# Optimization experiments

Measured on AMD Instinct MI355X. Metric: run time of the kernel, lower is better.

Reference implementation:

```python
import jax, jax.numpy as jnp
import numpy as np

B_, I_, H_ = 4096, 2048, 2048


def setup_inputs() -> dict:
    key = jax.random.key(0)
    ks = jax.random.split(key, 7)
    x = jax.random.normal(ks[0], (B_, I_), dtype=jnp.float32)
    h = jax.random.normal(ks[1], (B_, H_), dtype=jnp.float32)
    c = jax.random.normal(ks[2], (B_, H_), dtype=jnp.float32)
    n = jax.random.uniform(ks[3], (B_, H_), dtype=jnp.float32)  # positive normalizer state
    m = jax.random.normal(ks[4], (B_, H_), dtype=jnp.float32)
    # xavier_uniform over [I+H, 4H]
    fan_in, fan_out = I_ + H_, 4 * H_
    limit = float(np.sqrt(6.0 / (fan_in + fan_out)))
    W = jax.random.uniform(ks[5], (fan_in, fan_out), dtype=jnp.float32, minval=-limit, maxval=limit)
    Bias = jnp.zeros((fan_out,), dtype=jnp.float32)
    return {"x": x, "h": h, "c": c, "n": n, "m": m, "W": W, "Bias": Bias}


def reference(x, h, c, n, m, W, Bias):
    H = h.shape[1]
    combined = jnp.concatenate([x, h], axis=1)            # [B, I+H]
    gates = combined @ W + Bias                           # [B, 4H]
    z_tilda, i_tilda, f_tilda, o_tilda = jnp.split(gates, 4, axis=1)
    z_t = jnp.tanh(z_tilda)
    f_t = jax.nn.sigmoid(f_tilda)
    o_t = jax.nn.sigmoid(o_tilda)
    # log(sigmoid(f_tilda)) == log_sigmoid(f_tilda); log(exp(i_tilda)) == i_tilda
    m_t = jnp.maximum(jax.nn.log_sigmoid(f_tilda) + m, i_tilda)
    i_prime = jnp.exp(i_tilda - m_t)
    c_t = f_t * c + i_prime * z_t
    n_t = f_t * n + i_prime
    h_t = o_t * (c_t / n_t)
    return jnp.stack([h_t, c_t, n_t, m_t])  # [4, B, H]
```

## Files before the change

kernel.cpp:

```cpp
#include <hip/hip_runtime.h>
#include <hip/hip_fp16.h>

#define B_SZ 4096
#define I_SZ 2048
#define H_SZ 2048
#define K_SZ 4096
#define N_SZ 8192

typedef _Float16 half8_t __attribute__((ext_vector_type(8)));
typedef _Float16 half4_t __attribute__((ext_vector_type(4)));
typedef float    f32x4   __attribute__((ext_vector_type(4)));

typedef const void __attribute__((address_space(1)))* gas_ptr;
typedef void       __attribute__((address_space(3)))* las_ptr;

__device__ __forceinline__ void async_load16(const void* g, void* l) {
    __builtin_amdgcn_global_load_lds((gas_ptr)g, (las_ptr)l, 16, 0, 0);
}

__global__ void cast_combined_kernel(const float* __restrict__ x,
                                     const float* __restrict__ h,
                                     _Float16* __restrict__ A) {
    int idx = blockIdx.x * 256 + threadIdx.x;
    int b   = idx >> 10;
    int c4  = idx & 1023;
    const float* src = (c4 < 512) ? (x + (size_t)b * I_SZ + c4 * 4)
                                  : (h + (size_t)b * H_SZ + (c4 - 512) * 4);
    f32x4 v = *(const f32x4*)src;
    half4_t o = { (_Float16)v[0], (_Float16)v[1], (_Float16)v[2], (_Float16)v[3] };
    *(half4_t*)(A + (size_t)b * K_SZ + c4 * 4) = o;
}

__global__ void transpose_cast_W(const float* __restrict__ W,
                                 _Float16* __restrict__ Wt) {
    __shared__ _Float16 tile[64][65];
    int nt = blockIdx.x;
    int kt = blockIdx.y;
    int tx = threadIdx.x & 63;
    int tg = threadIdx.x >> 6;
#pragma unroll
    for (int r = 0; r < 16; ++r) {
        int kl = r * 4 + tg;
        float v = W[(size_t)(kt * 64 + kl) * N_SZ + nt * 64 + tx];
        tile[kl][tx] = (_Float16)v;
    }
    __syncthreads();
#pragma unroll
    for (int r = 0; r < 16; ++r) {
        int nl = r * 4 + tg;
        Wt[(size_t)(nt * 64 + nl) * K_SZ + kt * 64 + tx] = tile[tx][nl];
    }
}

__global__ __launch_bounds__(256)
void gemm_kernel(const _Float16* __restrict__ A,
                 const _Float16* __restrict__ Wt,
                 float* __restrict__ G) {
    __shared__ _Float16 sA[128 * 32];
    __shared__ _Float16 sB[128 * 32];
    const int t    = threadIdx.x;
    const int wave = t >> 6;
    const int lane = t & 63;
    const int m0 = blockIdx.y * 128;
    const int n0 = blockIdx.x * 128;
    const int wm = (wave >> 1) * 64;
    const int wn = (wave & 1) * 64;

    f32x4 acc[4][4] = {};

    const int srow = wave * 16 + (lane >> 2);
    const int scol = (lane & 3) * 8;
    const _Float16* gA0 = A  + (size_t)(m0 + srow) * K_SZ + scol;
    const _Float16* gB0 = Wt + (size_t)(n0 + srow) * K_SZ + scol;
    char* lA = (char*)sA + wave * 1024;
    char* lB = (char*)sB + wave * 1024;

    const int lm = lane & 15;
    const int kq = (lane >> 4) * 8;

    for (int k0 = 0; k0 < K_SZ; k0 += 32) {
        async_load16(gA0 + k0,             lA);
        async_load16(gA0 + 64 * K_SZ + k0, lA + 4096);
        async_load16(gB0 + k0,             lB);
        async_load16(gB0 + 64 * K_SZ + k0, lB + 4096);
        __syncthreads();

        half8_t af[4], bf[4];
#pragma unroll
        for (int i = 0; i < 4; ++i)
            af[i] = *(const half8_t*)(sA + (wm + i * 16 + lm) * 32 + kq);
#pragma unroll
        for (int i = 0; i < 4; ++i)
            bf[i] = *(const half8_t*)(sB + (wn + i * 16 + lm) * 32 + kq);
#pragma unroll
        for (int mi = 0; mi < 4; ++mi)
#pragma unroll
            for (int ni = 0; ni < 4; ++ni)
                acc[mi][ni] = __builtin_amdgcn_mfma_f32_16x16x32_f16(
                    af[mi], bf[ni], acc[mi][ni], 0, 0, 0);
        __syncthreads();
    }

    const int cr = (lane >> 4) * 4;
    const int cc = lane & 15;
#pragma unroll
    for (int mi = 0; mi < 4; ++mi)
#pragma unroll
        for (int ni = 0; ni < 4; ++ni)
#pragma unroll
            for (int r = 0; r < 4; ++r) {
                int row = m0 + wm + mi * 16 + cr + r;
                int col = n0 + wn + ni * 16 + cc;
                G[(size_t)row * N_SZ + col] = acc[mi][ni][r];
            }
}

__global__ void eltwise_kernel(const float* __restrict__ G,
                               const float* __restrict__ Bias,
                               const float* __restrict__ c,
                               const float* __restrict__ n,
                               const float* __restrict__ m,
                               float* __restrict__ out) {
    const size_t BH = (size_t)B_SZ * H_SZ;
    int idx = blockIdx.x * 256 + threadIdx.x;
    int b  = idx >> 9;
    int j4 = (idx & 511) * 4;
    const float* gr = G + (size_t)b * N_SZ;
    f32x4 zt = *(const f32x4*)(gr + j4);
    f32x4 it = *(const f32x4*)(gr + H_SZ + j4);
    f32x4 ft = *(const f32x4*)(gr + 2 * H_SZ + j4);
    f32x4 ot = *(const f32x4*)(gr + 3 * H_SZ + j4);
    f32x4 bz = *(const f32x4*)(Bias + j4);
    f32x4 bi = *(const f32x4*)(Bias + H_SZ + j4);
    f32x4 bf = *(const f32x4*)(Bias + 2 * H_SZ + j4);
    f32x4 bo = *(const f32x4*)(Bias + 3 * H_SZ + j4);
    f32x4 cv = *(const f32x4*)(c + (size_t)b * H_SZ + j4);
    f32x4 nv = *(const f32x4*)(n + (size_t)b * H_SZ + j4);
    f32x4 mv = *(const f32x4*)(m + (size_t)b * H_SZ + j4);
    f32x4 hR, cR, nR, mR;
#pragma unroll
    for (int q = 0; q < 4; ++q) {
        float z  = zt[q] + bz[q];
        float i  = it[q] + bi[q];
        float f  = ft[q] + bf[q];
        float o  = ot[q] + bo[q];
        float z_t = tanhf(z);
        float f_t = 1.0f / (1.0f + expf(-f));
        float o_t = 1.0f / (1.0f + expf(-o));
        float ls  = fminf(f, 0.0f) - log1pf(expf(-fabsf(f)));
        float m_t = fmaxf(ls + mv[q], i);
        float ip  = expf(i - m_t);
        float c_t = f_t * cv[q] + ip * z_t;
        float n_t = f_t * nv[q] + ip;
        float h_t = o_t * (c_t / n_t);
        hR[q] = h_t; cR[q] = c_t; nR[q] = n_t; mR[q] = m_t;
    }
    size_t off = (size_t)b * H_SZ + j4;
    *(f32x4*)(out + off)          = hR;
    *(f32x4*)(out + BH + off)     = cR;
    *(f32x4*)(out + 2 * BH + off) = nR;
    *(f32x4*)(out + 3 * BH + off) = mR;
}

extern "C" void kernel_launch(void* const* d_in, const int* in_sizes, int n_in,
                              void* d_out, int out_size, void* d_ws, size_t ws_size,
                              hipStream_t stream) {
    const float* x    = (const float*)d_in[0];
    const float* h    = (const float*)d_in[1];
    const float* c    = (const float*)d_in[2];
    const float* n    = (const float*)d_in[3];
    const float* m    = (const float*)d_in[4];
    const float* W    = (const float*)d_in[5];
    const float* Bias = (const float*)d_in[6];
    float* out = (float*)d_out;

    const size_t WT_BYTES = (size_t)N_SZ * K_SZ * 2;
    const size_t A_BYTES  = (size_t)B_SZ * K_SZ * 2;
    const size_t G_BYTES  = (size_t)B_SZ * N_SZ * 4;
    if (ws_size < WT_BYTES + A_BYTES + G_BYTES) return;

    char* ws = (char*)d_ws;
    _Float16* Wt = (_Float16*)ws;
    _Float16* A  = (_Float16*)(ws + WT_BYTES);
    float*    G  = (float*)(ws + WT_BYTES + A_BYTES);

    cast_combined_kernel<<<16384, 256, 0, stream>>>(x, h, A);
    transpose_cast_W<<<dim3(128, 64), 256, 0, stream>>>(W, Wt);
    gemm_kernel<<<dim3(64, 32), 256, 0, stream>>>(A, Wt, G);
    eltwise_kernel<<<8192, 256, 0, stream>>>(G, Bias, c, n, m, out);
}
```

Measured before the change: 813.3 us.

## Fuse LSTM gate epilogue into GEMM with gate-interleaved tiles and swizzled LDS

Each GEMM block now computes the z/i/f/o gate columns for the same 32 hidden units, so the elementwise xLSTM update runs in the GEMM epilogue. This removes the fp32 gates buffer write and re-read and the separate elementwise launch. It also XOR-swizzles the LDS layout to reduce bank conflicts and switches to fast hardware exp2/rcp/log intrinsics, which lowers precision slightly. The W transpose kernel is simplified to a direct strided gather with 8-wide fp16 stores; its uncoalesced reads may cost more than the old shared-memory tile version.

```diff
diff --git a/kernel.cpp b/kernel.cpp
--- a/kernel.cpp
+++ b/kernel.cpp
@@ -1,7 +1,7 @@
 #include <hip/hip_runtime.h>
 #include <hip/hip_fp16.h>
 
-#define B_SZ 4096
+#define M_SZ 4096
 #define I_SZ 2048
 #define H_SZ 2048
 #define K_SZ 4096
@@ -16,6 +16,14 @@
 
 __device__ __forceinline__ void async_load16(const void* g, void* l) {
     __builtin_amdgcn_global_load_lds((gas_ptr)g, (las_ptr)l, 16, 0, 0);
+}
+
+__device__ __forceinline__ float fexp(float x) {
+    return __builtin_amdgcn_exp2f(x * 1.44269504088896340736f);
+}
+__device__ __forceinline__ float frcp(float x) { return __builtin_amdgcn_rcpf(x); }
+__device__ __forceinline__ float flog1p(float t) {
+    return __builtin_amdgcn_logf(1.0f + t) * 0.69314718055994530942f;
 }
 
 __global__ void cast_combined_kernel(const float* __restrict__ x,
@@ -33,69 +41,73 @@
 
 __global__ void transpose_cast_W(const float* __restrict__ W,
                                  _Float16* __restrict__ Wt) {
-    __shared__ _Float16 tile[64][65];
-    int nt = blockIdx.x;
-    int kt = blockIdx.y;
-    int tx = threadIdx.x & 63;
-    int tg = threadIdx.x >> 6;
+    int t  = threadIdx.x;
+    int n  = blockIdx.x * 64 + (t >> 2);
+    int k0 = blockIdx.y * 32 + (t & 3) * 8;
+    half8_t v;
 #pragma unroll
-    for (int r = 0; r < 16; ++r) {
-        int kl = r * 4 + tg;
-        float v = W[(size_t)(kt * 64 + kl) * N_SZ + nt * 64 + tx];
-        tile[kl][tx] = (_Float16)v;
-    }
-    __syncthreads();
-#pragma unroll
-    for (int r = 0; r < 16; ++r) {
-        int nl = r * 4 + tg;
-        Wt[(size_t)(nt * 64 + nl) * K_SZ + kt * 64 + tx] = tile[tx][nl];
-    }
+    for (int j = 0; j < 8; ++j)
+        v[j] = (_Float16)W[(size_t)(k0 + j) * N_SZ + n];
+    *(half8_t*)(Wt + (size_t)n * K_SZ + k0) = v;
 }
 
 __global__ __launch_bounds__(256)
-void gemm_kernel(const _Float16* __restrict__ A,
-                 const _Float16* __restrict__ Wt,
-                 float* __restrict__ G) {
+void gemm_fused_kernel(const _Float16* __restrict__ A,
+                       const _Float16* __restrict__ Wt,
+                       const float* __restrict__ Bias,
+                       const float* __restrict__ Cst,
+                       const float* __restrict__ Nst,
+                       const float* __restrict__ Mst,
+                       float* __restrict__ out) {
     __shared__ _Float16 sA[128 * 32];
     __shared__ _Float16 sB[128 * 32];
     const int t    = threadIdx.x;
     const int wave = t >> 6;
     const int lane = t & 63;
     const int m0 = blockIdx.y * 128;
-    const int n0 = blockIdx.x * 128;
-    const int wm = (wave >> 1) * 64;
-    const int wn = (wave & 1) * 64;
+    const int j0 = blockIdx.x * 32;
 
-    f32x4 acc[4][4] = {};
+    f32x4 acc[2][8] = {};
 
-    const int srow = wave * 16 + (lane >> 2);
-    const int scol = (lane & 3) * 8;
-    const _Float16* gA0 = A  + (size_t)(m0 + srow) * K_SZ + scol;
-    const _Float16* gB0 = Wt + (size_t)(n0 + srow) * K_SZ + scol;
-    char* lA = (char*)sA + wave * 1024;
-    char* lB = (char*)sB + wave * 1024;
+    const int srl   = lane >> 2;
+    const int chunk = (lane & 3) ^ ((lane >> 3) & 3);
+    const int ar0 = wave * 16 + srl;
+    const int br0 = wave * 16 + srl;
+    const int br1 = br0 + 64;
+    const int wrow0 = (br0 >> 5) * H_SZ + j0 + (br0 & 31);
+    const int wrow1 = (br1 >> 5) * H_SZ + j0 + (br1 & 31);
 
-    const int lm = lane & 15;
-    const int kq = (lane >> 4) * 8;
+    const _Float16* gA0 = A  + (size_t)(m0 + ar0) * K_SZ + chunk * 8;
+    const _Float16* gA1 = gA0 + (size_t)64 * K_SZ;
+    const _Float16* gB0 = Wt + (size_t)wrow0 * K_SZ + chunk * 8;
+    const _Float16* gB1 = Wt + (size_t)wrow1 * K_SZ + chunk * 8;
+    char* lA0 = (char*)sA + wave * 1024;
+    char* lA1 = lA0 + 4096;
+    char* lB0 = (char*)sB + wave * 1024;
+    char* lB1 = lB0 + 4096;
+
+    const int lm   = lane & 15;
+    const int slot = (lane >> 4) ^ ((lm >> 1) & 3);
+    const _Float16* fA = sA + (wave * 32 + lm) * 32 + slot * 8;
+    const _Float16* fB = sB + lm * 32 + slot * 8;
 
     for (int k0 = 0; k0 < K_SZ; k0 += 32) {
-        async_load16(gA0 + k0,             lA);
-        async_load16(gA0 + 64 * K_SZ + k0, lA + 4096);
-        async_load16(gB0 + k0,             lB);
-        async_load16(gB0 + 64 * K_SZ + k0, lB + 4096);
+        async_load16(gA0 + k0, lA0);
+        async_load16(gA1 + k0, lA1);
+        async_load16(gB0 + k0, lB0);
+        async_load16(gB1 + k0, lB1);
         __syncthreads();
 
-        half8_t af[4], bf[4];
+        half8_t af[2], bf[8];
+        af[0] = *(const half8_t*)(fA);
+        af[1] = *(const half8_t*)(fA + 16 * 32);
 #pragma unroll
-        for (int i = 0; i < 4; ++i)
-            af[i] = *(const half8_t*)(sA + (wm + i * 16 + lm) * 32 + kq);
+        for (int ni = 0; ni < 8; ++ni)
+            bf[ni] = *(const half8_t*)(fB + ni * 16 * 32);
 #pragma unroll
-        for (int i = 0; i < 4; ++i)
-            bf[i] = *(const half8_t*)(sB + (wn + i * 16 + lm) * 32 + kq);
+        for (int mi = 0; mi < 2; ++mi)
 #pragma unroll
-        for (int mi = 0; mi < 4; ++mi)
-#pragma unroll
-            for (int ni = 0; ni < 4; ++ni)
+            for (int ni = 0; ni < 8; ++ni)
                 acc[mi][ni] = __builtin_amdgcn_mfma_f32_16x16x32_f16(
                     af[mi], bf[ni], acc[mi][ni], 0, 0, 0);
         __syncthreads();
@@ -103,63 +115,40 @@
 
     const int cr = (lane >> 4) * 4;
     const int cc = lane & 15;
+    const size_t bh = (size_t)M_SZ * H_SZ;
 #pragma unroll
-    for (int mi = 0; mi < 4; ++mi)
+    for (int mi = 0; mi < 2; ++mi) {
 #pragma unroll
-        for (int ni = 0; ni < 4; ++ni)
+        for (int nj = 0; nj < 2; ++nj) {
+            const int j = j0 + nj * 16 + cc;
+            const float bz = Bias[j];
+            const float bi = Bias[H_SZ + j];
+            const float bff = Bias[2 * H_SZ + j];
+            const float bo = Bias[3 * H_SZ + j];
 #pragma unroll
             for (int r = 0; r < 4; ++r) {
-                int row = m0 + wm + mi * 16 + cr + r;
-                int col = n0 + wn + ni * 16 + cc;
-                G[(size_t)row * N_SZ + col] = acc[mi][ni][r];
+                const int m = m0 + wave * 32 + mi * 16 + cr + r;
+                const size_t off = (size_t)m * H_SZ + j;
+                float z = acc[mi][nj][r]     + bz;
+                float i = acc[mi][2 + nj][r] + bi;
+                float f = acc[mi][4 + nj][r] + bff;
+                float o = acc[mi][6 + nj][r] + bo;
+                float z_t = 1.0f - 2.0f * frcp(fexp(2.0f * z) + 1.0f);
+                float f_t = frcp(1.0f + fexp(-f));
+                float o_t = frcp(1.0f + fexp(-o));
+                float ls  = fminf(f, 0.0f) - flog1p(fexp(-fabsf(f)));
+                float m_t = fmaxf(ls + Mst[off], i);
+                float ip  = fexp(i - m_t);
+                float c_t = f_t * Cst[off] + ip * z_t;
+                float n_t = f_t * Nst[off] + ip;
+                float h_t = o_t * c_t * frcp(n_t);
+                out[off]          = h_t;
+                out[bh + off]     = c_t;
+                out[2 * bh + off] = n_t;
+                out[3 * bh + off] = m_t;
             }
-}
-
-__global__ void eltwise_kernel(const float* __restrict__ G,
-                               const float* __restrict__ Bias,
-                               const float* __restrict__ c,
-                               const float* __restrict__ n,
-                               const float* __restrict__ m,
-                               float* __restrict__ out) {
-    const size_t BH = (size_t)B_SZ * H_SZ;
-    int idx = blockIdx.x * 256 + threadIdx.x;
-    int b  = idx >> 9;
-    int j4 = (idx & 511) * 4;
-    const float* gr = G + (size_t)b * N_SZ;
-    f32x4 zt = *(const f32x4*)(gr + j4);
-    f32x4 it = *(const f32x4*)(gr + H_SZ + j4);
-    f32x4 ft = *(const f32x4*)(gr + 2 * H_SZ + j4);
-    f32x4 ot = *(const f32x4*)(gr + 3 * H_SZ + j4);
-    f32x4 bz = *(const f32x4*)(Bias + j4);
-    f32x4 bi = *(const f32x4*)(Bias + H_SZ + j4);
-    f32x4 bf = *(const f32x4*)(Bias + 2 * H_SZ + j4);
-    f32x4 bo = *(const f32x4*)(Bias + 3 * H_SZ + j4);
-    f32x4 cv = *(const f32x4*)(c + (size_t)b * H_SZ + j4);
-    f32x4 nv = *(const f32x4*)(n + (size_t)b * H_SZ + j4);
-    f32x4 mv = *(const f32x4*)(m + (size_t)b * H_SZ + j4);
-    f32x4 hR, cR, nR, mR;
-#pragma unroll
-    for (int q = 0; q < 4; ++q) {
-        float z  = zt[q] + bz[q];
-        float i  = it[q] + bi[q];
-        float f  = ft[q] + bf[q];
-        float o  = ot[q] + bo[q];
-        float z_t = tanhf(z);
-        float f_t = 1.0f / (1.0f + expf(-f));
-        float o_t = 1.0f / (1.0f + expf(-o));
-        float ls  = fminf(f, 0.0f) - log1pf(expf(-fabsf(f)));
-        float m_t = fmaxf(ls + mv[q], i);
-        float ip  = expf(i - m_t);
-        float c_t = f_t * cv[q] + ip * z_t;
-        float n_t = f_t * nv[q] + ip;
-        float h_t = o_t * (c_t / n_t);
-        hR[q] = h_t; cR[q] = c_t; nR[q] = n_t; mR[q] = m_t;
+        }
     }
-    size_t off = (size_t)b * H_SZ + j4;
-    *(f32x4*)(out + off)          = hR;
-    *(f32x4*)(out + BH + off)     = cR;
-    *(f32x4*)(out + 2 * BH + off) = nR;
-    *(f32x4*)(out + 3 * BH + off) = mR;
 }
 
 extern "C" void kernel_launch(void* const* d_in, const int* in_sizes, int n_in,
@@ -175,17 +164,14 @@
     float* out = (float*)d_out;
 
     const size_t WT_BYTES = (size_t)N_SZ * K_SZ * 2;
-    const size_t A_BYTES  = (size_t)B_SZ * K_SZ * 2;
-    const size_t G_BYTES  = (size_t)B_SZ * N_SZ * 4;
-    if (ws_size < WT_BYTES + A_BYTES + G_BYTES) return;
+    const size_t A_BYTES  = (size_t)M_SZ * K_SZ * 2;
+    if (ws_size < WT_BYTES + A_BYTES) return;
 
     char* ws = (char*)d_ws;
     _Float16* Wt = (_Float16*)ws;
     _Float16* A  = (_Float16*)(ws + WT_BYTES);
-    float*    G  = (float*)(ws + WT_BYTES + A_BYTES);
 
     cast_combined_kernel<<<16384, 256, 0, stream>>>(x, h, A);
-    transpose_cast_W<<<dim3(128, 64), 256, 0, stream>>>(W, Wt);
-    gemm_kernel<<<dim3(64, 32), 256, 0, stream>>>(A, Wt, G);
-    eltwise_kernel<<<8192, 256, 0, stream>>>(G, Bias, c, n, m, out);
+    transpose_cast_W<<<dim3(128, 128), 256, 0, stream>>>(W, Wt);
+    gemm_fused_kernel<<<dim3(64, 32), 256, 0, stream>>>(A, Wt, Bias, c, n, m, out);
 }
```

After: 747.4 us. 1.09x faster.
